# Kernel tuning notes

Hardware: AMD Instinct MI355X
Metric: run time of the kernel (lower is better)

The kernel has to match this reference:

```python
import jax, jax.numpy as jnp
import numpy as np
import math

B, T, D, H = 2, 2048, 1024, 16


def _layernorm(x, gamma, beta, eps=1e-5):
    mu = jnp.mean(x, axis=-1, keepdims=True)
    var = jnp.var(x, axis=-1, keepdims=True)
    return (x - mu) * jax.lax.rsqrt(var + eps) * gamma + beta


def setup_inputs() -> dict:
    key = jax.random.key(0)
    ks = jax.random.split(key, 12)
    s = 1.0 / math.sqrt(D)
    return {
        "x": jax.random.normal(ks[0], (B, T, D), dtype=jnp.float32),
        "src_mask": jax.random.randint(ks[1], (B, T, T), 0, 2, dtype=jnp.int32),
        "ln_gamma": jnp.ones((D,), jnp.float32),
        "ln_beta": jnp.zeros((D,), jnp.float32),
        "Wq": jax.random.normal(ks[2], (D, D), jnp.float32) * s,
        "bq": jnp.zeros((D,), jnp.float32),
        "Wk": jax.random.normal(ks[3], (D, D), jnp.float32) * s,
        "bk": jnp.zeros((D,), jnp.float32),
        "Wv": jax.random.normal(ks[4], (D, D), jnp.float32) * s,
        "bv": jnp.zeros((D,), jnp.float32),
        "Wo": jax.random.normal(ks[5], (D, D), jnp.float32) * s,
        "bo": jnp.zeros((D,), jnp.float32),
    }


def reference(x, src_mask, ln_gamma, ln_beta, Wq, bq, Wk, bk, Wv, bv, Wo, bo):
    Bx, Tx, Dx = x.shape
    dh = Dx // H
    xn = _layernorm(x, ln_gamma, ln_beta)  # single LN; the three calls are identical
    q = (xn @ Wq + bq).reshape(Bx, Tx, H, dh)
    k = (xn @ Wk + bk).reshape(Bx, Tx, H, dh)
    v = (xn @ Wv + bv).reshape(Bx, Tx, H, dh)
    # scores: B, n, m, h
    attn = jnp.einsum('bnhd,bmhd->bnmh', q, k) / math.sqrt(dh)
    attn = attn + (1.0 - src_mask.astype(attn.dtype))[..., None] * -100000.0
    weight = jax.nn.softmax(attn, axis=2)
    y = jnp.einsum('bnmh,bmhd->bnhd', weight, v).reshape(Bx, Tx, Dx)
    return x + (y @ Wo + bo)
```

## Files before the change

kernel.cpp:

```cpp
#include <hip/hip_runtime.h>
#include <hip/hip_bf16.h>
#include <stdint.h>

#define Tq 2048
#define Dd 1024
#define Hh 16

typedef unsigned short u16;
typedef __attribute__((ext_vector_type(8))) short short8;
typedef __attribute__((ext_vector_type(4))) float f32x4;

__device__ __forceinline__ u16 f2bf(float f) {
  union { float f; unsigned u; } v; v.f = f;
  unsigned r = (v.u + 0x7fffu + ((v.u >> 16) & 1u)) >> 16;
  return (u16)r;
}

__device__ __forceinline__ unsigned pk2bf(float a, float b) {
  __hip_bfloat162 h = __float22bfloat162_rn(float2{a, b});
  union { __hip_bfloat162 h; unsigned u; } c; c.h = h;
  return c.u;
}

__device__ __forceinline__ void load_lds16(const void* g, void* l) {
  __builtin_amdgcn_global_load_lds(
      (const __attribute__((address_space(1))) unsigned*)g,
      (__attribute__((address_space(3))) unsigned*)l, 16, 0, 0);
}

__device__ __forceinline__ f32x4 mfma16(short8 a, short8 b, f32x4 c) {
  return __builtin_amdgcn_mfma_f32_16x16x32_bf16(a, b, c, 0, 0, 0);
}

__global__ __launch_bounds__(256) void prep_kernel(
    const float* __restrict__ x, const float* __restrict__ gamma,
    const float* __restrict__ beta, u16* __restrict__ xn,
    const float* __restrict__ W0, const float* __restrict__ W1,
    const float* __restrict__ W2, const float* __restrict__ W3,
    u16* __restrict__ o_qkv, u16* __restrict__ o_o,
    const int* __restrict__ mask, uint32_t* __restrict__ bits,
    const float* __restrict__ bq, const float* __restrict__ bk,
    const float* __restrict__ bv, float* __restrict__ bias3) {
  __shared__ float t[32][33];
  int idx = blockIdx.x;
  int tid = threadIdx.x;
  if (idx < 4096) {
    int row = idx;
    const float4 v = ((const float4*)(x + (size_t)row * Dd))[tid];
    float s = v.x + v.y + v.z + v.w;
    float s2 = v.x * v.x + v.y * v.y + v.z * v.z + v.w * v.w;
#pragma unroll
    for (int off = 1; off < 64; off <<= 1) {
      s += __shfl_xor(s, off);
      s2 += __shfl_xor(s2, off);
    }
    int w = tid >> 6;
    if ((tid & 63) == 0) { t[0][w] = s; t[0][4 + w] = s2; }
    __syncthreads();
    s = t[0][0] + t[0][1] + t[0][2] + t[0][3];
    s2 = t[0][4] + t[0][5] + t[0][6] + t[0][7];
    float mu = s * (1.0f / Dd);
    float var = s2 * (1.0f / Dd) - mu * mu;
    float rstd = rsqrtf(var + 1e-5f);
    const float4 g = ((const float4*)gamma)[tid];
    const float4 bb = ((const float4*)beta)[tid];
    union { unsigned us[2]; uint2 u2; } o;
    o.us[0] = pk2bf((v.x - mu) * rstd * g.x + bb.x, (v.y - mu) * rstd * g.y + bb.y);
    o.us[1] = pk2bf((v.z - mu) * rstd * g.z + bb.z, (v.w - mu) * rstd * g.w + bb.w);
    *(uint2*)(xn + (size_t)row * Dd + tid * 4) = o.u2;
  } else if (idx < 8192) {
    int ti = idx - 4096;
    int z = ti >> 10, i = ti & 1023;
    const float* W = (z == 0) ? W0 : (z == 1) ? W1 : (z == 2) ? W2 : W3;
    u16* out = (z < 3) ? (o_qkv + (size_t)z * 1024 * 1024) : o_o;
    int k0 = (i & 31) * 32, n0 = (i >> 5) * 32;
    int tx = tid & 31, ty = tid >> 5;
#pragma unroll
    for (int j = 0; j < 4; ++j)
      t[ty + j * 8][tx] = W[(size_t)(k0 + ty + j * 8) * Dd + n0 + tx];
    __syncthreads();
#pragma unroll
    for (int j = 0; j < 4; ++j)
      out[(size_t)(n0 + ty + j * 8) * Dd + k0 + tx] = f2bf(t[tx][ty + j * 8]);
  } else if (idx < 9216) {
    int m = idx - 8192;
    int b = m >> 9, rest = m & 511;
    int qw = rest >> 3, kblk = rest & 7;
    int k = kblk * 256 + tid;
    const int* mp = mask + ((size_t)b * Tq + qw * 32) * Tq + k;
    uint32_t wv = 0;
#pragma unroll
    for (int j = 0; j < 32; ++j) wv |= (mp[(size_t)j * Tq] ? 1u : 0u) << j;
    bits[((size_t)b * 64 + qw) * Tq + k] = wv;
  } else {
    int i = (idx - 9216) * 256 + tid;
    float v = (i < 1024) ? bq[i] : (i < 2048) ? bk[i - 1024] : bv[i - 2048];
    bias3[i] = v;
  }
}

__global__ __launch_bounds__(256) void vt_kernel(
    const u16* __restrict__ qkv, u16* __restrict__ vt) {
  __shared__ u16 t[32][33];
  int bh = blockIdx.z;
  int b = bh >> 4, h = bh & 15;
  int t0 = blockIdx.x * 32, d0 = blockIdx.y * 32;
  int tx = threadIdx.x & 31, ty = threadIdx.x >> 5;
#pragma unroll
  for (int i = 0; i < 4; ++i)
    t[ty + i * 8][tx] =
        qkv[(size_t)(b * Tq + t0 + ty + i * 8) * 3072 + 2048 + h * 64 + d0 + tx];
  __syncthreads();
#pragma unroll
  for (int i = 0; i < 4; ++i)
    vt[((size_t)bh * 64 + d0 + ty + i * 8) * Tq + t0 + tx] = t[tx][ty + i * 8];
}

template <int MODE, int MT>
__global__ __launch_bounds__(256) void gemm_bt(
    const u16* __restrict__ A, const u16* __restrict__ Bt,
    const float* __restrict__ bias, const float* __restrict__ resid,
    void* __restrict__ Cout, int ldc, int K) {
  constexpr int MTI = MT / 32;
  constexpr int ACALLS = MT / 64;
  __shared__ u16 As[MT * 32];
  __shared__ u16 Bs[128 * 32];
  int tid = threadIdx.x;
  int lane = tid & 63, w = tid >> 6;
  int l16 = lane & 15, quad = lane >> 4;
  int wm = w >> 1, wn = w & 1;
  int m0 = blockIdx.y * MT, n0 = blockIdx.x * 128;
  int srow = lane >> 2, scol = (lane & 3) << 3;
  const u16* ga0 = A + (size_t)(m0 + srow) * K + scol;
  const u16* gb0 = Bt + (size_t)(n0 + srow) * K + scol;
  f32x4 acc[MTI][4];
#pragma unroll
  for (int i = 0; i < MTI; ++i)
#pragma unroll
    for (int j = 0; j < 4; ++j) acc[i][j] = {0.f, 0.f, 0.f, 0.f};

  for (int k0 = 0; k0 < K; k0 += 32) {
    __syncthreads();
#pragma unroll
    for (int c = 0; c < ACALLS; ++c) {
      int rb = w * (MT / 4) + c * 16;
      load_lds16(ga0 + (size_t)rb * K + k0, (char*)As + rb * 64);
    }
#pragma unroll
    for (int c = 0; c < 2; ++c) {
      int rb = w * 32 + c * 16;
      load_lds16(gb0 + (size_t)rb * K + k0, (char*)Bs + rb * 64);
    }
    __syncthreads();
    short8 af[MTI], bf[4];
#pragma unroll
    for (int mt = 0; mt < MTI; ++mt)
      af[mt] = *(const short8*)&As[(wm * (MT / 2) + mt * 16 + l16) * 32 + quad * 8];
#pragma unroll
    for (int nt = 0; nt < 4; ++nt)
      bf[nt] = *(const short8*)&Bs[(wn * 64 + nt * 16 + l16) * 32 + quad * 8];
#pragma unroll
    for (int mt = 0; mt < MTI; ++mt)
#pragma unroll
      for (int nt = 0; nt < 4; ++nt)
        acc[mt][nt] = mfma16(af[mt], bf[nt], acc[mt][nt]);
  }
#pragma unroll
  for (int nt = 0; nt < 4; ++nt) {
    int col = n0 + wn * 64 + nt * 16 + l16;
    float bv = bias[col];
    float scl = (MODE == 0 && col < 1024) ? 0.125f : 1.0f;
#pragma unroll
    for (int mt = 0; mt < MTI; ++mt) {
#pragma unroll
      for (int r = 0; r < 4; ++r) {
        int row = m0 + wm * (MT / 2) + mt * 16 + quad * 4 + r;
        size_t idx = (size_t)row * ldc + col;
        float vv = (acc[mt][nt][r] + bv) * scl;
        if (MODE == 0)
          ((u16*)Cout)[idx] = f2bf(vv);
        else
          ((float*)Cout)[idx] = vv + resid[idx];
      }
    }
  }
}

__global__ __launch_bounds__(256, 2) void attn_kernel(
    const u16* __restrict__ qkv, const u16* __restrict__ vt,
    const uint32_t* __restrict__ mbits, u16* __restrict__ ybuf) {
  __shared__ u16 Ks[2][64 * 64];
  __shared__ u16 Vs[2][64 * 64];
  __shared__ u16 Plds[4][32 * 64];
  int tid = threadIdx.x;
  int lane = tid & 63, w = tid >> 6;
  int l16 = lane & 15, quad = lane >> 4;
  int x7 = l16 & 7;
  int qt = blockIdx.x, h = blockIdx.y, b = blockIdx.z;
  int qbase = qt * 128 + w * 32;
  const u16* Qb = qkv + (size_t)b * Tq * 3072 + h * 64;
  const u16* Kb = Qb + 1024;
  const u16* Vb = vt + ((size_t)(b * Hh + h)) * 64 * Tq;
  const uint32_t* Mrow = mbits + ((size_t)b * 64 + (qbase >> 5)) * Tq;
  u16* Pw = Plds[w];

  int half = (w & 1) * 32;
  int r8 = lane >> 3;
  int phys = lane & 7;
  int chunk = phys ^ r8;
  bool isK = (w < 2);

  short8 qf[2][2];
#pragma unroll
  for (int nt = 0; nt < 2; ++nt)
#pragma unroll
    for (int ks = 0; ks < 2; ++ks)
      qf[nt][ks] = *(const short8*)&Qb[(size_t)(qbase + nt * 16 + l16) * 3072 +
                                       ks * 32 + quad * 8];

  f32x4 acc[2][4];
#pragma unroll
  for (int i = 0; i < 2; ++i)
#pragma unroll
    for (int j = 0; j < 4; ++j) acc[i][j] = {0.f, 0.f, 0.f, 0.f};
  float lst[2] = {0.f, 0.f};

  auto stage = [&](int buf, int k0) {
    if (isK) {
#pragma unroll
      for (int j = 0; j < 4; ++j)
        load_lds16(Kb + (size_t)(k0 + half + j * 8 + r8) * 3072 + chunk * 8,
                   (char*)&Ks[buf][0] + (half + j * 8) * 128);
    } else {
#pragma unroll
      for (int j = 0; j < 4; ++j)
        load_lds16(Vb + (size_t)(half + j * 8 + r8) * Tq + k0 + chunk * 8,
                   (char*)&Vs[buf][0] + (half + j * 8) * 128);
    }
  };

  stage(0, 0);

  for (int kt = 0; kt < 32; ++kt) {
    int k0 = kt * 64;
    int buf = kt & 1;
    __syncthreads();
    uint32_t mv[4][4];
#pragma unroll
    for (int mt = 0; mt < 4; ++mt) {
      uint4 m4 = *(const uint4*)&Mrow[k0 + mt * 16 + quad * 4];
      mv[mt][0] = m4.x; mv[mt][1] = m4.y; mv[mt][2] = m4.z; mv[mt][3] = m4.w;
    }
    if (kt < 31) stage(buf ^ 1, k0 + 64);
    const u16* Kt = Ks[buf];
    const u16* Vtile = Vs[buf];
    f32x4 s[4][2];
#pragma unroll
    for (int i = 0; i < 4; ++i)
#pragma unroll
      for (int j = 0; j < 2; ++j) s[i][j] = {0.f, 0.f, 0.f, 0.f};
#pragma unroll
    for (int mt = 0; mt < 4; ++mt)
#pragma unroll
      for (int ks = 0; ks < 2; ++ks) {
        short8 kf = *(const short8*)&Kt[(mt * 16 + l16) * 64 +
                                        (((ks << 2) | quad) ^ x7) * 8];
#pragma unroll
        for (int nt = 0; nt < 2; ++nt)
          s[mt][nt] = mfma16(kf, qf[nt][ks], s[mt][nt]);
      }
#pragma unroll
    for (int nt = 0; nt < 2; ++nt) {
      int shift = nt * 16 + l16;
#pragma unroll
      for (int mt = 0; mt < 4; ++mt) {
#pragma unroll
        for (int r = 0; r < 4; ++r) {
          float sv = ((mv[mt][r] >> shift) & 1u) ? s[mt][nt][r] : -100000.0f;
          float p = __expf(sv);
          s[mt][nt][r] = p;
          lst[nt] += p;
        }
        union { unsigned us[2]; uint2 u2; } pk;
        pk.us[0] = pk2bf(s[mt][nt][0], s[mt][nt][1]);
        pk.us[1] = pk2bf(s[mt][nt][2], s[mt][nt][3]);
        int p16 = (mt * 2 + (quad >> 1)) ^ x7;
        *(uint2*)&Pw[(nt * 16 + l16) * 64 + p16 * 8 + (quad & 1) * 4] = pk.u2;
      }
    }
    short8 pf[2][2];
#pragma unroll
    for (int mt2 = 0; mt2 < 2; ++mt2)
#pragma unroll
      for (int ks = 0; ks < 2; ++ks)
        pf[mt2][ks] = *(const short8*)&Pw[(mt2 * 16 + l16) * 64 +
                                          (((ks << 2) | quad) ^ x7) * 8];
#pragma unroll
    for (int ks = 0; ks < 2; ++ks)
#pragma unroll
      for (int nt2 = 0; nt2 < 4; ++nt2) {
        short8 vf = *(const short8*)&Vtile[(nt2 * 16 + l16) * 64 +
                                           (((ks << 2) | quad) ^ x7) * 8];
#pragma unroll
        for (int mt2 = 0; mt2 < 2; ++mt2)
          acc[mt2][nt2] = mfma16(pf[mt2][ks], vf, acc[mt2][nt2]);
      }
  }
#pragma unroll
  for (int nt = 0; nt < 2; ++nt) {
    lst[nt] += __shfl_xor(lst[nt], 16);
    lst[nt] += __shfl_xor(lst[nt], 32);
  }
#pragma unroll
  for (int mt2 = 0; mt2 < 2; ++mt2)
#pragma unroll
    for (int r = 0; r < 4; ++r) {
      float li = 1.0f / __shfl(lst[mt2], quad * 4 + r);
      size_t row = (size_t)b * Tq + qbase + mt2 * 16 + quad * 4 + r;
#pragma unroll
      for (int nt2 = 0; nt2 < 4; ++nt2)
        ybuf[row * Dd + h * 64 + nt2 * 16 + l16] = f2bf(acc[mt2][nt2][r] * li);
    }
}

extern "C" void kernel_launch(void* const* d_in, const int* in_sizes, int n_in,
                              void* d_out, int out_size, void* d_ws, size_t ws_size,
                              hipStream_t stream) {
  (void)in_sizes; (void)n_in; (void)out_size; (void)ws_size;
  const float* x = (const float*)d_in[0];
  const int* mask = (const int*)d_in[1];
  const float* gamma = (const float*)d_in[2];
  const float* beta = (const float*)d_in[3];
  const float* Wq = (const float*)d_in[4];
  const float* bq = (const float*)d_in[5];
  const float* Wk = (const float*)d_in[6];
  const float* bk = (const float*)d_in[7];
  const float* Wv = (const float*)d_in[8];
  const float* bv = (const float*)d_in[9];
  const float* Wo = (const float*)d_in[10];
  const float* bo = (const float*)d_in[11];
  float* out = (float*)d_out;
  char* ws = (char*)d_ws;

  constexpr size_t SZ_XN = (size_t)4096 * 1024 * 2;
  constexpr size_t SZ_WTQ = (size_t)3072 * 1024 * 2;
  constexpr size_t SZ_WOT = (size_t)1024 * 1024 * 2;
  constexpr size_t SZ_B3 = 3072 * 4;
  constexpr size_t SZ_QKV = (size_t)4096 * 3072 * 2;
  constexpr size_t SZ_MBITS = (size_t)2 * 64 * 2048 * 4;
  constexpr size_t SZ_VT = (size_t)2 * 16 * 64 * 2048 * 2;
  size_t off = 0;
  u16* xn = (u16*)(ws + off); off += SZ_XN;
  u16* wtqkv = (u16*)(ws + off); off += SZ_WTQ;
  u16* wot = (u16*)(ws + off); off += SZ_WOT;
  float* bias3 = (float*)(ws + off); off += SZ_B3;
  u16* qkvb = (u16*)(ws + off); off += SZ_QKV;
  uint32_t* mbits = (uint32_t*)(ws + off); off += SZ_MBITS;
  u16* vtb = (u16*)(ws + off); off += SZ_VT;
  u16* ybuf = (u16*)(ws + off);

  prep_kernel<<<dim3(9228), dim3(256), 0, stream>>>(
      x, gamma, beta, xn, Wq, Wk, Wv, Wo, wtqkv, wot, mask, mbits, bq, bk, bv,
      bias3);
  gemm_bt<0, 128><<<dim3(24, 32), dim3(256), 0, stream>>>(
      xn, wtqkv, bias3, nullptr, qkvb, 3072, 1024);
  vt_kernel<<<dim3(64, 2, 32), dim3(256), 0, stream>>>(qkvb, vtb);
  attn_kernel<<<dim3(16, 16, 2), dim3(256), 0, stream>>>(qkvb, vtb, mbits, ybuf);
  gemm_bt<1, 64><<<dim3(8, 64), dim3(256), 0, stream>>>(
      ybuf, wot, bo, x, out, 1024, 1024);
}
```

Measured before the change: 246.0 us.

## Deepen GEMM K-tile with swizzled LDS, halve attention query tile, use exp2

The GEMM now stages 64-wide K tiles into XOR-swizzled LDS, halving the number of barrier pairs per K loop and avoiding bank conflicts on fragment reads. The attention kernel gives each wave 16 queries instead of 32, doubles the grid and raises the occupancy hint to 4 blocks per CU to hide latency better, at the cost of loading each K/V tile twice as often. The softmax switches to exp2f, with log2(e) folded into the Q scale in the GEMM epilogue, so the exponential becomes cheaper.

```diff
diff --git a/kernel.cpp b/kernel.cpp
--- a/kernel.cpp
+++ b/kernel.cpp
@@ -122,54 +122,66 @@
     const float* __restrict__ bias, const float* __restrict__ resid,
     void* __restrict__ Cout, int ldc, int K) {
   constexpr int MTI = MT / 32;
-  constexpr int ACALLS = MT / 64;
-  __shared__ u16 As[MT * 32];
-  __shared__ u16 Bs[128 * 32];
+  __shared__ u16 As[MT * 64];
+  __shared__ u16 Bs[128 * 64];
   int tid = threadIdx.x;
   int lane = tid & 63, w = tid >> 6;
   int l16 = lane & 15, quad = lane >> 4;
+  int x7 = l16 & 7;
   int wm = w >> 1, wn = w & 1;
   int m0 = blockIdx.y * MT, n0 = blockIdx.x * 128;
-  int srow = lane >> 2, scol = (lane & 3) << 3;
-  const u16* ga0 = A + (size_t)(m0 + srow) * K + scol;
-  const u16* gb0 = Bt + (size_t)(n0 + srow) * K + scol;
+  int r8 = lane >> 3;
+  int phys = lane & 7;
+  int chunk = phys ^ r8;
+  const u16* ga0 = A + (size_t)(m0 + r8) * K + chunk * 8;
+  const u16* gb0 = Bt + (size_t)(n0 + r8) * K + chunk * 8;
   f32x4 acc[MTI][4];
 #pragma unroll
   for (int i = 0; i < MTI; ++i)
 #pragma unroll
     for (int j = 0; j < 4; ++j) acc[i][j] = {0.f, 0.f, 0.f, 0.f};
 
-  for (int k0 = 0; k0 < K; k0 += 32) {
-    __syncthreads();
-#pragma unroll
-    for (int c = 0; c < ACALLS; ++c) {
-      int rb = w * (MT / 4) + c * 16;
-      load_lds16(ga0 + (size_t)rb * K + k0, (char*)As + rb * 64);
-    }
-#pragma unroll
-    for (int c = 0; c < 2; ++c) {
-      int rb = w * 32 + c * 16;
-      load_lds16(gb0 + (size_t)rb * K + k0, (char*)Bs + rb * 64);
-    }
-    __syncthreads();
-    short8 af[MTI], bf[4];
-#pragma unroll
-    for (int mt = 0; mt < MTI; ++mt)
-      af[mt] = *(const short8*)&As[(wm * (MT / 2) + mt * 16 + l16) * 32 + quad * 8];
-#pragma unroll
-    for (int nt = 0; nt < 4; ++nt)
-      bf[nt] = *(const short8*)&Bs[(wn * 64 + nt * 16 + l16) * 32 + quad * 8];
-#pragma unroll
-    for (int mt = 0; mt < MTI; ++mt)
-#pragma unroll
-      for (int nt = 0; nt < 4; ++nt)
-        acc[mt][nt] = mfma16(af[mt], bf[nt], acc[mt][nt]);
+  for (int k0 = 0; k0 < K; k0 += 64) {
+    __syncthreads();
+#pragma unroll
+    for (int c = 0; c < MT / 32; ++c) {
+      int rb = c * 32 + w * 8;
+      load_lds16(ga0 + (size_t)rb * K + k0, (char*)As + rb * 128);
+    }
+#pragma unroll
+    for (int c = 0; c < 4; ++c) {
+      int rb = c * 32 + w * 8;
+      load_lds16(gb0 + (size_t)rb * K + k0, (char*)Bs + rb * 128);
+    }
+    __syncthreads();
+    short8 af[MTI][2], bf[4][2];
+#pragma unroll
+    for (int mt = 0; mt < MTI; ++mt) {
+      int row = wm * (MT / 2) + mt * 16 + l16;
+#pragma unroll
+      for (int ks = 0; ks < 2; ++ks)
+        af[mt][ks] = *(const short8*)&As[row * 64 + (((ks << 2) | quad) ^ x7) * 8];
+    }
+#pragma unroll
+    for (int nt = 0; nt < 4; ++nt) {
+      int row = wn * 64 + nt * 16 + l16;
+#pragma unroll
+      for (int ks = 0; ks < 2; ++ks)
+        bf[nt][ks] = *(const short8*)&Bs[row * 64 + (((ks << 2) | quad) ^ x7) * 8];
+    }
+#pragma unroll
+    for (int ks = 0; ks < 2; ++ks)
+#pragma unroll
+      for (int mt = 0; mt < MTI; ++mt)
+#pragma unroll
+        for (int nt = 0; nt < 4; ++nt)
+          acc[mt][nt] = mfma16(af[mt][ks], bf[nt][ks], acc[mt][nt]);
   }
 #pragma unroll
   for (int nt = 0; nt < 4; ++nt) {
     int col = n0 + wn * 64 + nt * 16 + l16;
     float bv = bias[col];
-    float scl = (MODE == 0 && col < 1024) ? 0.125f : 1.0f;
+    float scl = (MODE == 0 && col < 1024) ? 0.18033688011112042f : 1.0f;
 #pragma unroll
     for (int mt = 0; mt < MTI; ++mt) {
 #pragma unroll
@@ -186,22 +198,23 @@
   }
 }
 
-__global__ __launch_bounds__(256, 2) void attn_kernel(
+__global__ __launch_bounds__(256, 4) void attn_kernel(
     const u16* __restrict__ qkv, const u16* __restrict__ vt,
     const uint32_t* __restrict__ mbits, u16* __restrict__ ybuf) {
   __shared__ u16 Ks[2][64 * 64];
   __shared__ u16 Vs[2][64 * 64];
-  __shared__ u16 Plds[4][32 * 64];
+  __shared__ u16 Plds[4][16 * 64];
   int tid = threadIdx.x;
   int lane = tid & 63, w = tid >> 6;
   int l16 = lane & 15, quad = lane >> 4;
   int x7 = l16 & 7;
   int qt = blockIdx.x, h = blockIdx.y, b = blockIdx.z;
-  int qbase = qt * 128 + w * 32;
+  int qbase = qt * 64 + w * 16;
   const u16* Qb = qkv + (size_t)b * Tq * 3072 + h * 64;
   const u16* Kb = Qb + 1024;
   const u16* Vb = vt + ((size_t)(b * Hh + h)) * 64 * Tq;
   const uint32_t* Mrow = mbits + ((size_t)b * 64 + (qbase >> 5)) * Tq;
+  int shift = (w & 1) * 16 + l16;
   u16* Pw = Plds[w];
 
   int half = (w & 1) * 32;
@@ -210,20 +223,15 @@
   int chunk = phys ^ r8;
   bool isK = (w < 2);
 
-  short8 qf[2][2];
-#pragma unroll
-  for (int nt = 0; nt < 2; ++nt)
-#pragma unroll
-    for (int ks = 0; ks < 2; ++ks)
-      qf[nt][ks] = *(const short8*)&Qb[(size_t)(qbase + nt * 16 + l16) * 3072 +
-                                       ks * 32 + quad * 8];
-
-  f32x4 acc[2][4];
-#pragma unroll
-  for (int i = 0; i < 2; ++i)
-#pragma unroll
-    for (int j = 0; j < 4; ++j) acc[i][j] = {0.f, 0.f, 0.f, 0.f};
-  float lst[2] = {0.f, 0.f};
+  short8 qf[2];
+#pragma unroll
+  for (int ks = 0; ks < 2; ++ks)
+    qf[ks] = *(const short8*)&Qb[(size_t)(qbase + l16) * 3072 + ks * 32 + quad * 8];
+
+  f32x4 acc[4];
+#pragma unroll
+  for (int j = 0; j < 4; ++j) acc[j] = {0.f, 0.f, 0.f, 0.f};
+  float lst = 0.f;
 
   auto stage = [&](int buf, int k0) {
     if (isK) {
@@ -254,73 +262,55 @@
     if (kt < 31) stage(buf ^ 1, k0 + 64);
     const u16* Kt = Ks[buf];
     const u16* Vtile = Vs[buf];
-    f32x4 s[4][2];
-#pragma unroll
-    for (int i = 0; i < 4; ++i)
-#pragma unroll
-      for (int j = 0; j < 2; ++j) s[i][j] = {0.f, 0.f, 0.f, 0.f};
+    f32x4 s[4];
+#pragma unroll
+    for (int i = 0; i < 4; ++i) s[i] = {0.f, 0.f, 0.f, 0.f};
 #pragma unroll
     for (int mt = 0; mt < 4; ++mt)
 #pragma unroll
       for (int ks = 0; ks < 2; ++ks) {
         short8 kf = *(const short8*)&Kt[(mt * 16 + l16) * 64 +
                                         (((ks << 2) | quad) ^ x7) * 8];
-#pragma unroll
-        for (int nt = 0; nt < 2; ++nt)
-          s[mt][nt] = mfma16(kf, qf[nt][ks], s[mt][nt]);
+        s[mt] = mfma16(kf, qf[ks], s[mt]);
       }
 #pragma unroll
-    for (int nt = 0; nt < 2; ++nt) {
-      int shift = nt * 16 + l16;
-#pragma unroll
-      for (int mt = 0; mt < 4; ++mt) {
-#pragma unroll
-        for (int r = 0; r < 4; ++r) {
-          float sv = ((mv[mt][r] >> shift) & 1u) ? s[mt][nt][r] : -100000.0f;
-          float p = __expf(sv);
-          s[mt][nt][r] = p;
-          lst[nt] += p;
-        }
-        union { unsigned us[2]; uint2 u2; } pk;
-        pk.us[0] = pk2bf(s[mt][nt][0], s[mt][nt][1]);
-        pk.us[1] = pk2bf(s[mt][nt][2], s[mt][nt][3]);
-        int p16 = (mt * 2 + (quad >> 1)) ^ x7;
-        *(uint2*)&Pw[(nt * 16 + l16) * 64 + p16 * 8 + (quad & 1) * 4] = pk.u2;
+    for (int mt = 0; mt < 4; ++mt) {
+#pragma unroll
+      for (int r = 0; r < 4; ++r) {
+        float sv = ((mv[mt][r] >> shift) & 1u) ? s[mt][r] : -100000.0f;
+        float p = exp2f(sv);
+        s[mt][r] = p;
+        lst += p;
       }
-    }
-    short8 pf[2][2];
-#pragma unroll
-    for (int mt2 = 0; mt2 < 2; ++mt2)
-#pragma unroll
-      for (int ks = 0; ks < 2; ++ks)
-        pf[mt2][ks] = *(const short8*)&Pw[(mt2 * 16 + l16) * 64 +
-                                          (((ks << 2) | quad) ^ x7) * 8];
+      union { unsigned us[2]; uint2 u2; } pk;
+      pk.us[0] = pk2bf(s[mt][0], s[mt][1]);
+      pk.us[1] = pk2bf(s[mt][2], s[mt][3]);
+      int p16 = (mt * 2 + (quad >> 1)) ^ x7;
+      *(uint2*)&Pw[l16 * 64 + p16 * 8 + (quad & 1) * 4] = pk.u2;
+    }
+    short8 pf[2];
+#pragma unroll
+    for (int ks = 0; ks < 2; ++ks)
+      pf[ks] = *(const short8*)&Pw[l16 * 64 + (((ks << 2) | quad) ^ x7) * 8];
 #pragma unroll
     for (int ks = 0; ks < 2; ++ks)
 #pragma unroll
       for (int nt2 = 0; nt2 < 4; ++nt2) {
         short8 vf = *(const short8*)&Vtile[(nt2 * 16 + l16) * 64 +
                                            (((ks << 2) | quad) ^ x7) * 8];
-#pragma unroll
-        for (int mt2 = 0; mt2 < 2; ++mt2)
-          acc[mt2][nt2] = mfma16(pf[mt2][ks], vf, acc[mt2][nt2]);
+        acc[nt2] = mfma16(pf[ks], vf, acc[nt2]);
       }
   }
-#pragma unroll
-  for (int nt = 0; nt < 2; ++nt) {
-    lst[nt] += __shfl_xor(lst[nt], 16);
-    lst[nt] += __shfl_xor(lst[nt], 32);
-  }
-#pragma unroll
-  for (int mt2 = 0; mt2 < 2; ++mt2)
-#pragma unroll
-    for (int r = 0; r < 4; ++r) {
-      float li = 1.0f / __shfl(lst[mt2], quad * 4 + r);
-      size_t row = (size_t)b * Tq + qbase + mt2 * 16 + quad * 4 + r;
-#pragma unroll
-      for (int nt2 = 0; nt2 < 4; ++nt2)
-        ybuf[row * Dd + h * 64 + nt2 * 16 + l16] = f2bf(acc[mt2][nt2][r] * li);
-    }
+  lst += __shfl_xor(lst, 16);
+  lst += __shfl_xor(lst, 32);
+#pragma unroll
+  for (int r = 0; r < 4; ++r) {
+    float li = 1.0f / __shfl(lst, quad * 4 + r);
+    size_t row = (size_t)b * Tq + qbase + quad * 4 + r;
+#pragma unroll
+    for (int nt2 = 0; nt2 < 4; ++nt2)
+      ybuf[row * Dd + h * 64 + nt2 * 16 + l16] = f2bf(acc[nt2][r] * li);
+  }
 }
 
 extern "C" void kernel_launch(void* const* d_in, const int* in_sizes, int n_in,
@@ -365,7 +355,7 @@
   gemm_bt<0, 128><<<dim3(24, 32), dim3(256), 0, stream>>>(
       xn, wtqkv, bias3, nullptr, qkvb, 3072, 1024);
   vt_kernel<<<dim3(64, 2, 32), dim3(256), 0, stream>>>(qkvb, vtb);
-  attn_kernel<<<dim3(16, 16, 2), dim3(256), 0, stream>>>(qkvb, vtb, mbits, ybuf);
+  attn_kernel<<<dim3(32, 16, 2), dim3(256), 0, stream>>>(qkvb, vtb, mbits, ybuf);
   gemm_bt<1, 64><<<dim3(8, 64), dim3(256), 0, stream>>>(
       ybuf, wot, bo, x, out, 1024, 1024);
 }
```

Result: no change. 248.3 us (+0.9%).
